# Kernel tuning notes

Hardware: AMD Instinct MI355X
Metric: run time of the kernel (lower is better)

## Reference

```python
import jax, jax.numpy as jnp
import numpy as np

SEQ_LEN = 256
E = 1024      # embedding_dim (= decoder LSTM hidden size)
H = 2048      # encoder hidden_dim
LAT = 512     # latent_space_dim
CLS = 512     # common_latent_space_dim
MIX = 384     # mixture_size
VJ = 64       # embedding_dim_VJ  (constraint: 2*VJ + LAT + MIX == E)
ALPH = 32; NVG = 64; NJG = 16
X_IDX = 0; B_IDX = 1  # indices of 'X' (start) and 'B' (stop) letters


def _lstm_final(xs, h0, c0, Wih, Whh, bih, bhh):
    """Run an LSTM over xs [T, B, in] and return the final hidden state [B, H]."""
    def step(carry, x):
        h, c = carry
        g = x @ Wih.T + bih + h @ Whh.T + bhh
        i, f, gg, o = jnp.split(g, 4, axis=-1)
        c = jax.nn.sigmoid(f) * c + jax.nn.sigmoid(i) * jnp.tanh(gg)
        h = jax.nn.sigmoid(o) * jnp.tanh(c)
        return (h, c), None
    (h, c), _ = jax.lax.scan(step, (h0, c0), xs)
    return h


def _decode(h0c, Wih, Whh, bih, bhh, start_vec, end_vec, n_steps):
    """Autoregressive LSTM decode: feed previous output back as next input.
    h0c [1,E] is used as both initial h and c (as in the source)."""
    def step(carry, _):
        h, c, prev = carry
        g = prev @ Wih.T + bih + h @ Whh.T + bhh
        i, f, gg, o = jnp.split(g, 4, axis=-1)
        c2 = jax.nn.sigmoid(f) * c + jax.nn.sigmoid(i) * jnp.tanh(gg)
        h2 = jax.nn.sigmoid(o) * jnp.tanh(c2)
        return (h2, c2, h2), h2
    _, ys = jax.lax.scan(step, (h0c, h0c, start_vec), None, length=n_steps)  # [T-2,1,E]
    seq = jnp.concatenate([start_vec[None], ys, end_vec[None]], axis=0)      # [T,1,E]
    return seq[::-1]  # source reverses the list before cat


def setup_inputs() -> dict:
    key = jax.random.key(0)
    ks = jax.random.split(key, 26)
    def g(k, shape):
        return jax.random.normal(k, shape, dtype=jnp.float32) * 0.05
    return {
        "x": jax.random.randint(ks[0], (SEQ_LEN,), 0, ALPH),
        "Vg": jax.random.randint(ks[1], (1,), 0, NVG),
        "Jg": jax.random.randint(ks[2], (1,), 0, NJG),
        "emb": g(ks[3], (ALPH, E)),
        "emb_Vg": g(ks[4], (NVG, VJ)),
        "emb_Jg": g(ks[5], (NJG, VJ)),
        "enc_Wih": g(ks[6], (4 * H, E)),
        "enc_Whh": g(ks[7], (4 * H, H)),
        "enc_bih": g(ks[8], (4 * H,)),
        "enc_bhh": g(ks[9], (4 * H,)),
        "cls_W": g(ks[10], (CLS, 2 * H)), "cls_b": g(ks[11], (CLS,)),
        "latf_W": g(ks[12], (LAT, H)), "latf_b": g(ks[13], (LAT,)),
        "latr_W": g(ks[14], (LAT, H)), "latr_b": g(ks[15], (LAT,)),
        "mix_W": g(ks[16], (MIX, CLS)), "mix_b": g(ks[17], (MIX,)),
        "recf_Wih": g(ks[18], (4 * E, E)), "recf_Whh": g(ks[19], (4 * E, E)),
        "recf_bih": g(ks[20], (4 * E,)), "recf_bhh": g(ks[21], (4 * E,)),
        "recr_Wih": g(ks[22], (4 * E, E)), "recr_Whh": g(ks[23], (4 * E, E)),
        "recr_bih": g(ks[24], (4 * E,)), "recr_bhh": g(ks[25], (4 * E,)),
    }


def reference(x, Vg, Jg, emb, emb_Vg, emb_Jg,
              enc_Wih, enc_Whh, enc_bih, enc_bhh,
              cls_W, cls_b, latf_W, latf_b, latr_W, latr_b,
              mix_W, mix_b,
              recf_Wih, recf_Whh, recf_bih, recf_bhh,
              recr_Wih, recr_Whh, recr_bih, recr_bhh):
    T = x.shape[0]
    emb_f = emb[x]          # [T, E]
    emb_r = emb_f[::-1]     # reversed sequence
    h0 = jnp.zeros((1, H), jnp.float32)
    # NB: the source (bug preserved) runs the reverse pass through lstm_in_f as well.
    hf = _lstm_final(emb_f[:, None, :], h0, h0, enc_Wih, enc_Whh, enc_bih, enc_bhh)  # [1,H]
    hr = _lstm_final(emb_r[:, None, :], h0, h0, enc_Wih, enc_Whh, enc_bih, enc_bhh)  # [1,H]
    # dropout treated in eval mode (identity) for a deterministic reference
    common = jnp.tanh(jnp.concatenate([hf, hr], axis=-1) @ cls_W.T + cls_b)  # [1,CLS]
    lat_f = hf @ latf_W.T + latf_b  # [1,LAT]
    lat_r = hr @ latr_W.T + latr_b
    vg = emb_Vg[Vg]  # [1,VJ]
    jg = emb_Jg[Jg]
    lat_f_full = jnp.concatenate([vg, lat_f, jg], axis=-1)  # [1, 2*VJ+LAT]
    lat_r_full = jnp.concatenate([vg, lat_r, jg], axis=-1)
    # source (bug preserved): mixture_to_f applied to both branches
    mix = common @ mix_W.T + mix_b                      # [1,MIX]
    h0f = jnp.concatenate([lat_f_full, mix], axis=-1)   # [1,E]
    h0r = jnp.concatenate([lat_r_full, mix], axis=-1)
    start = emb[X_IDX][None]  # 'X' embedding, [1,E]
    stop = emb[B_IDX][None]   # 'B' embedding
    rec_f = _decode(h0f, recf_Wih, recf_Whh, recf_bih, recf_bhh, start, stop, T - 2)
    rec_r = _decode(h0r, recr_Wih, recr_Whh, recr_bih, recr_bhh, stop, start, T - 2)
    return (lat_f_full[None], lat_r_full[None], rec_f, rec_r, emb_f, emb_r)
```

## Files before the change

### kernel.cpp

```cpp
#include <hip/hip_runtime.h>
#include <hip/hip_fp16.h>

#define NB 256
#define NT 512


struct KArgs {
  const int *x, *Vg, *Jg;
  const float *emb, *embVg, *embJg;
  const float *encWih, *encWhh, *encBih, *encBhh;
  const float *clsW, *clsB, *latfW, *latfB, *latrW, *latrB, *mixW, *mixB;
  const float *recWih[2], *recWhh[2], *recBih[2], *recBhh[2];
  float* out;
  unsigned* barFull;
  unsigned long long *eDat, *hTdec;
  float *common, *bsum, *d1, *embf, *P;
  unsigned short *Wcomb, *WhhE;
  int fast;
};

__device__ __forceinline__ unsigned packh2(float lo, float hi) {
  __half2 h = __floats2half2_rn(lo, hi);
  return *(unsigned*)&h;
}
__device__ __forceinline__ float2 h2f2(unsigned u) {
  __half2 h = *(__half2*)&u;
  return __half22float2(h);
}
__device__ __forceinline__ unsigned long long packtag(unsigned tag, float f) {
  return ((unsigned long long)tag << 32) | (unsigned long long)__float_as_uint(f);
}
__device__ __forceinline__ float sigm(float x) { return 1.f / (1.f + __expf(-x)); }
__device__ __forceinline__ float tanh_(float x) { return 2.f / (1.f + __expf(-2.f * x)) - 1.f; }
__device__ __forceinline__ float wred(float v) {
#pragma unroll
  for (int off = 32; off; off >>= 1) v += __shfl_xor(v, off, 64);
  return v;
}
__device__ __forceinline__ void cstoref(float* p, float v) {
  __hip_atomic_store(p, v, __ATOMIC_RELAXED, __HIP_MEMORY_SCOPE_AGENT);
}
__device__ __forceinline__ float cloadf(const float* p) {
  return __hip_atomic_load(p, __ATOMIC_RELAXED, __HIP_MEMORY_SCOPE_AGENT);
}
__device__ __forceinline__ void cstoreu(unsigned* p, unsigned v) {
  __hip_atomic_store(p, v, __ATOMIC_RELAXED, __HIP_MEMORY_SCOPE_AGENT);
}
__device__ __forceinline__ unsigned long long cload64(const unsigned long long* p) {
  return __hip_atomic_load(p, __ATOMIC_RELAXED, __HIP_MEMORY_SCOPE_AGENT);
}
__device__ __forceinline__ void cstore64(unsigned long long* p, unsigned long long v) {
  __hip_atomic_store(p, v, __ATOMIC_RELAXED, __HIP_MEMORY_SCOPE_AGENT);
}

__device__ __forceinline__ void gbar_tree(unsigned* tree, int idx, unsigned e) {
  const int ls = 8;
  __syncthreads();
  if (threadIdx.x == 0) {
    unsigned* leaf = tree + (idx >> 3) * ls;
    unsigned* root = tree + 32 * ls;
    unsigned* flag = root + ls;
    unsigned old = __hip_atomic_fetch_add(leaf, 1u, __ATOMIC_ACQ_REL, __HIP_MEMORY_SCOPE_AGENT);
    if (old == e * 8u - 1u) {
      unsigned ro = __hip_atomic_fetch_add(root, 1u, __ATOMIC_ACQ_REL, __HIP_MEMORY_SCOPE_AGENT);
      if (ro == e * 32u - 1u)
        __hip_atomic_store(flag, e, __ATOMIC_RELEASE, __HIP_MEMORY_SCOPE_AGENT);
    }
    while (__hip_atomic_load(flag, __ATOMIC_RELAXED, __HIP_MEMORY_SCOPE_AGENT) < e)
      __builtin_amdgcn_s_sleep(2);
    __builtin_amdgcn_fence(__ATOMIC_ACQUIRE, "agent");
  }
  __syncthreads();
}

__global__ __launch_bounds__(NT, 2) void rnn2_kernel(KArgs a) {
  __shared__ float smem[16384];
  const int tid = threadIdx.x;
  const int b = blockIdx.x;
  const int wq = __builtin_amdgcn_readfirstlane(tid >> 6);
  const int lane = tid & 63;

  float* out_recf = a.out + 1280;
  float* out_recr = a.out + 1280 + 262144;
  float* out_embf = a.out + 1280 + 2 * 262144;
  float* out_embr = a.out + 1280 + 3 * 262144;

  for (int i = tid; i < 2048; i += NT) smem[i] = a.emb[i];
  __syncthreads();
  {
    int wg = b * 8 + wq;
#pragma unroll 1
    for (int rr = 0; rr < 4; rr++) {
      int idx = wg + rr * 2048;
      int dir = idx >> 12;
      int row = idx & 4095;
      const float* Wih = a.recWih[dir];
      const float* sv = &smem[dir * 1024];
      float acc = 0.f;
#pragma unroll
      for (int kc = 0; kc < 4; kc++) {
        int k = kc * 256 + lane * 4;
        float4 wv = *(const float4*)&Wih[row * 1024 + k];
        float4 ev = *(const float4*)&sv[k];
        acc += wv.x * ev.x + wv.y * ev.y + wv.z * ev.z + wv.w * ev.w;
      }
      acc = wred(acc);
      if (lane == 0)
        cstoref(&a.d1[dir * 4096 + row], acc + a.recBih[dir][row] + a.recBhh[dir][row]);
    }
  }
  const int gtid = b * NT + tid;
  const int GSZ = NB * NT;
  for (int i = gtid; i < 256 * 1024; i += GSZ) {
    int t = i >> 10, e = i & 1023;
    float v = a.emb[a.x[t] * 1024 + e];
    cstoref(&a.embf[i], v);
    out_embf[i] = v;
    out_embr[(255 - t) * 1024 + e] = v;
  }
  if (gtid < 1024) {
    int e = gtid;
    out_recf[e] = a.emb[1024 + e];
    out_recf[255 * 1024 + e] = a.emb[e];
    out_recr[e] = a.emb[e];
    out_recr[255 * 1024 + e] = a.emb[1024 + e];
  }
  if (gtid < 2048) cstore64(&a.eDat[gtid], 0ULL);
  else if (gtid < 4096) cstore64(&a.eDat[gtid], 0x0000000100000001ULL);
  if (gtid < 4096) cstore64(&a.hTdec[gtid], packtag(0xFFFFFFFFu, 0.f));
  if (gtid < 8192) {
    int dir = gtid >> 12, r = gtid & 4095;
    cstoref(&a.bsum[gtid], a.recBih[dir][r] + a.recBhh[dir][r]);
  }
  if (a.fast) {
    unsigned* W32 = (unsigned*)a.WhhE;
    const int N4 = 8192 * 2048 / 4;
    for (int i = gtid; i < N4; i += GSZ) {
      float4 v = *(const float4*)&a.encWhh[(size_t)i * 4];
      cstoreu(&W32[i * 2], packh2(v.x, v.y));
      cstoreu(&W32[i * 2 + 1], packh2(v.z, v.w));
    }
    unsigned* C32 = (unsigned*)a.Wcomb;
    const int M4 = 4096 * 1024 / 4;
    for (int i = gtid; i < 2 * M4; i += GSZ) {
      int dir = (i >= M4) ? 1 : 0;
      int j = i - dir * M4;
      float4 va = *(const float4*)&a.recWih[dir][(size_t)j * 4];
      float4 vb = *(const float4*)&a.recWhh[dir][(size_t)j * 4];
      cstoreu(&C32[(size_t)dir * (M4 * 2) + j * 2], packh2(va.x + vb.x, va.y + vb.y));
      cstoreu(&C32[(size_t)dir * (M4 * 2) + j * 2 + 1], packh2(va.z + vb.z, va.w + vb.w));
    }
  }
  gbar_tree(a.barFull, b, 1u);

  {
    const int tdb = b & 7;
    const int rb = (b >> 3) * 256;
    const int td = tdb * 64 + lane;
    const int dirc = td >> 8;
    const int tcol = td & 255;
    float acc[2][16];
#pragma unroll
    for (int p = 0; p < 2; p++)
#pragma unroll
      for (int r = 0; r < 16; r++) acc[p][r] = 0.f;
    const int s_td = tid >> 3;
    const int s_j = tid & 7;
    int std_ = tdb * 64 + s_td;
    int st = std_ & 255;
    const float* s_esrc = &a.embf[((std_ >> 8) ? (255 - st) : st) * 1024];
#pragma unroll 1
    for (int kc = 0; kc < 4; kc++) {
      __syncthreads();
#pragma unroll
      for (int m = 0; m < 8; m++) {
        int kk = s_j * 32 + m * 4;
        float4 v = *(const float4*)&s_esrc[kc * 256 + kk];
        smem[(kk + 0) * 64 + s_td] = v.x;
        smem[(kk + 1) * 64 + s_td] = v.y;
        smem[(kk + 2) * 64 + s_td] = v.z;
        smem[(kk + 3) * 64 + s_td] = v.w;
      }
      __syncthreads();
#pragma unroll
      for (int p = 0; p < 2; p++) {
        int row0 = rb + wq * 32 + p * 16;
#pragma unroll 1
        for (int k4 = 0; k4 < 64; k4++) {
          float e0 = smem[(k4 * 4 + 0) * 64 + lane];
          float e1 = smem[(k4 * 4 + 1) * 64 + lane];
          float e2 = smem[(k4 * 4 + 2) * 64 + lane];
          float e3 = smem[(k4 * 4 + 3) * 64 + lane];
#pragma unroll
          for (int r = 0; r < 16; r++) {
            const float* wp = &a.encWih[(size_t)(row0 + r) * 1024 + kc * 256 + k4 * 4];
            float w0 = wp[0], w1 = wp[1], w2 = wp[2], w3 = wp[3];
            acc[p][r] = fmaf(e0, w0, fmaf(e1, w1, fmaf(e2, w2, fmaf(e3, w3, acc[p][r]))));
          }
        }
      }
    }
#pragma unroll
    for (int p = 0; p < 2; p++)
#pragma unroll
      for (int r = 0; r < 16; r++) {
        int row = rb + wq * 32 + p * 16 + r;
        float bias = a.encBih[row] + a.encBhh[row];
        cstoref(&a.P[(size_t)(dirc * 8192 + row) * 256 + tcol], acc[p][r] + bias);
      }
  }
  gbar_tree(a.barFull, b, 2u);

  {
    const int u = b * 8 + wq;
    float wreg[128];
    if (a.fast) {
      const unsigned long long* W64 = (const unsigned long long*)a.WhhE;
#pragma unroll
      for (int g = 0; g < 4; g++)
#pragma unroll
        for (int c = 0; c < 8; c++) {
          unsigned long long w = cload64(&W64[(size_t)(g * 2048 + u) * 512 + c * 64 + lane]);
          float2 f01 = h2f2((unsigned)w), f23 = h2f2((unsigned)(w >> 32));
          wreg[(g * 8 + c) * 4 + 0] = f01.x;
          wreg[(g * 8 + c) * 4 + 1] = f01.y;
          wreg[(g * 8 + c) * 4 + 2] = f23.x;
          wreg[(g * 8 + c) * 4 + 3] = f23.y;
        }
    }
    float cf = 0.f, cr = 0.f;
#pragma unroll 1
    for (int t = 0; t < 256; t++) {
      float pf[4], pr[4];
#pragma unroll
      for (int g = 0; g < 4; g++) {
        pf[g] = cloadf(&a.P[(size_t)(g * 2048 + u) * 256 + t]);
        pr[g] = cloadf(&a.P[(size_t)(8192 + g * 2048 + u) * 256 + t]);
      }
      {
        const unsigned long long* dp = a.eDat + (size_t)(t & 1) * 2048;
        const unsigned lo_e = (unsigned)t & 1u;
        const unsigned hi_e = ((unsigned)t >> 1) & 1u;
        unsigned long long v[4];
        for (;;) {
#pragma unroll
          for (int j = 0; j < 4; j++) v[j] = cload64(&dp[j * 512 + tid]);
          unsigned bad = 0;
#pragma unroll
          for (int j = 0; j < 4; j++)
            bad |= ((unsigned)v[j] ^ lo_e) | (((unsigned)(v[j] >> 32)) ^ hi_e);
          if (!(bad & 1u)) break;
          __builtin_amdgcn_s_sleep(1);
        }
#pragma unroll
        for (int j = 0; j < 4; j++) {
          smem[j * 512 + tid] = __uint_as_float((unsigned)v[j]);
          smem[2048 + j * 512 + tid] = __uint_as_float((unsigned)(v[j] >> 32));
        }
      }
      __syncthreads();
      float af[4] = {0, 0, 0, 0}, ar[4] = {0, 0, 0, 0};
      if (a.fast) {
#pragma unroll
        for (int c = 0; c < 8; c++) {
          float4 hf = *(const float4*)&smem[c * 256 + lane * 4];
          float4 hr = *(const float4*)&smem[2048 + c * 256 + lane * 4];
#pragma unroll
          for (int g = 0; g < 4; g++) {
            const int wb = (g * 8 + c) * 4;
            af[g] = fmaf(wreg[wb + 0], hf.x, fmaf(wreg[wb + 1], hf.y,
                    fmaf(wreg[wb + 2], hf.z, fmaf(wreg[wb + 3], hf.w, af[g]))));
            ar[g] = fmaf(wreg[wb + 0], hr.x, fmaf(wreg[wb + 1], hr.y,
                    fmaf(wreg[wb + 2], hr.z, fmaf(wreg[wb + 3], hr.w, ar[g]))));
          }
        }
      } else {
#pragma unroll 1
        for (int kc = 0; kc < 8; kc++) {
          int k = kc * 256 + lane * 4;
          float4 hf = *(const float4*)&smem[k];
          float4 hr = *(const float4*)&smem[2048 + k];
#pragma unroll
          for (int g = 0; g < 4; g++) {
            float4 wv = *(const float4*)&a.encWhh[(size_t)(g * 2048 + u) * 2048 + k];
            af[g] += wv.x * hf.x + wv.y * hf.y + wv.z * hf.z + wv.w * hf.w;
            ar[g] += wv.x * hr.x + wv.y * hr.y + wv.z * hr.z + wv.w * hr.w;
          }
        }
      }
#pragma unroll
      for (int g = 0; g < 4; g++) { af[g] = wred(af[g]); ar[g] = wred(ar[g]); }
      float gi = af[0] + pf[0], gf = af[1] + pf[1], gg = af[2] + pf[2], go = af[3] + pf[3];
      cf = sigm(gf) * cf + sigm(gi) * tanh_(gg);
      float hfv = sigm(go) * tanh_(cf);
      gi = ar[0] + pr[0]; gf = ar[1] + pr[1]; gg = ar[2] + pr[2]; go = ar[3] + pr[3];
      cr = sigm(gf) * cr + sigm(gi) * tanh_(gg);
      float hrv = sigm(go) * tanh_(cr);
      if (lane == 0) {
        unsigned tag = (unsigned)(t + 1);
        unsigned fa = (__float_as_uint(hfv) & ~1u) | (tag & 1u);
        unsigned fb = (__float_as_uint(hrv) & ~1u) | ((tag >> 1) & 1u);
        cstore64(&a.eDat[(size_t)((t + 1) & 1) * 2048 + u],
                 ((unsigned long long)fb << 32) | fa);
      }
      __syncthreads();
    }
  }

  if (b <= 192) {
    {
      const unsigned long long* dp = a.eDat;
      unsigned long long v[4];
      for (;;) {
#pragma unroll
        for (int j = 0; j < 4; j++) v[j] = cload64(&dp[j * 512 + tid]);
        unsigned bad = 0;
#pragma unroll
        for (int j = 0; j < 4; j++)
          bad |= (unsigned)v[j] | ((unsigned)(v[j] >> 32));
        if (!(bad & 1u)) break;
        __builtin_amdgcn_s_sleep(1);
      }
#pragma unroll
      for (int j = 0; j < 4; j++) {
        smem[j * 512 + tid] = __uint_as_float((unsigned)v[j]);
        smem[2048 + j * 512 + tid] = __uint_as_float((unsigned)(v[j] >> 32));
      }
    }
    __syncthreads();
    int wg = b * 8 + wq;
    if (wg < 512) {
      int r = wg;
      float acc = 0.f;
#pragma unroll 1
      for (int kc = 0; kc < 16; kc++) {
        int k = kc * 256 + lane * 4;
        float4 wv = *(const float4*)&a.clsW[(size_t)r * 4096 + k];
        float4 hv = *(const float4*)&smem[k];
        acc += wv.x * hv.x + wv.y * hv.y + wv.z * hv.z + wv.w * hv.w;
      }
      acc = wred(acc);
      if (lane == 0) cstoref(&a.common[r], tanh_(acc + a.clsB[r]));
    } else if (wg < 1024) {
      int r = wg - 512;
      float acc = 0.f;
#pragma unroll 1
      for (int kc = 0; kc < 8; kc++) {
        int k = kc * 256 + lane * 4;
        float4 wv = *(const float4*)&a.latfW[(size_t)r * 2048 + k];
        float4 hv = *(const float4*)&smem[k];
        acc += wv.x * hv.x + wv.y * hv.y + wv.z * hv.z + wv.w * hv.w;
      }
      acc = wred(acc);
      if (lane == 0) {
        float v = acc + a.latfB[r];
        cstore64(&a.hTdec[64 + r], packtag(0u, v));
        a.out[64 + r] = v;
      }
    } else if (wg < 1536) {
      int r = wg - 1024;
      float acc = 0.f;
#pragma unroll 1
      for (int kc = 0; kc < 8; kc++) {
        int k = kc * 256 + lane * 4;
        float4 wv = *(const float4*)&a.latrW[(size_t)r * 2048 + k];
        float4 hv = *(const float4*)&smem[2048 + k];
        acc += wv.x * hv.x + wv.y * hv.y + wv.z * hv.z + wv.w * hv.w;
      }
      acc = wred(acc);
      if (lane == 0) {
        float v = acc + a.latrB[r];
        cstore64(&a.hTdec[1024 + 64 + r], packtag(0u, v));
        a.out[640 + 64 + r] = v;
      }
    } else if (wg == 1536) {
      float v = a.embVg[a.Vg[0] * 64 + lane];
      cstore64(&a.hTdec[lane], packtag(0u, v));
      cstore64(&a.hTdec[1024 + lane], packtag(0u, v));
      a.out[lane] = v;
      a.out[640 + lane] = v;
    } else if (wg == 1537) {
      float v = a.embJg[a.Jg[0] * 64 + lane];
      cstore64(&a.hTdec[576 + lane], packtag(0u, v));
      cstore64(&a.hTdec[1024 + 576 + lane], packtag(0u, v));
      a.out[576 + lane] = v;
      a.out[640 + 576 + lane] = v;
    }
  }
  gbar_tree(a.barFull, b, 3u);
  if (b < 48) {
    int wg = b * 8 + wq;
    smem[tid] = cloadf(&a.common[tid]);
    __syncthreads();
    float acc = 0.f;
#pragma unroll
    for (int kc = 0; kc < 2; kc++) {
      int k = kc * 256 + lane * 4;
      float4 wv = *(const float4*)&a.mixW[(size_t)wg * 512 + k];
      float4 hv = *(const float4*)&smem[k];
      acc += wv.x * hv.x + wv.y * hv.y + wv.z * hv.z + wv.w * hv.w;
    }
    acc = wred(acc);
    if (lane == 0) {
      float v = acc + a.mixB[wg];
      cstore64(&a.hTdec[640 + wg], packtag(0u, v));
      cstore64(&a.hTdec[1024 + 640 + wg], packtag(0u, v));
    }
  }
  gbar_tree(a.barFull, b, 4u);

  {
    const int dir = b & 1;
    const int hidx = b >> 1;
    const int u = hidx * 8 + wq;
    float* outrec = dir ? out_recr : out_recf;
    float bs[4];
#pragma unroll
    for (int g = 0; g < 4; g++) bs[g] = cloadf(&a.bsum[dir * 4096 + g * 1024 + u]);
    float wd[64];
    if (a.fast) {
      const unsigned long long* C64 = (const unsigned long long*)a.Wcomb;
      const size_t dbase = (size_t)dir * (4096 * 1024 / 4);
#pragma unroll
      for (int g = 0; g < 4; g++)
#pragma unroll
        for (int c = 0; c < 4; c++) {
          unsigned long long w = cload64(&C64[dbase + (size_t)(g * 1024 + u) * 256 + c * 64 + lane]);
          float2 f01 = h2f2((unsigned)w), f23 = h2f2((unsigned)(w >> 32));
          wd[(g * 4 + c) * 4 + 0] = f01.x;
          wd[(g * 4 + c) * 4 + 1] = f01.y;
          wd[(g * 4 + c) * 4 + 2] = f23.x;
          wd[(g * 4 + c) * 4 + 3] = f23.y;
        }
    }
    float c = 0.f;
#pragma unroll 1
    for (int s = 1; s <= 254; s++) {
      {
        const unsigned long long* src = a.hTdec + ((s - 1) & 1) * 2048 + dir * 1024;
        const unsigned tg = (unsigned)(s - 1);
        unsigned long long v0, v1;
        for (;;) {
          v0 = cload64(&src[tid]);
          v1 = cload64(&src[512 + tid]);
          if ((((unsigned)(v0 >> 32)) ^ tg) == 0u && (((unsigned)(v1 >> 32)) ^ tg) == 0u) break;
          __builtin_amdgcn_s_sleep(1);
        }
        smem[tid] = __uint_as_float((unsigned)v0);
        smem[512 + tid] = __uint_as_float((unsigned)v1);
      }
      __syncthreads();
      float acc[4] = {0, 0, 0, 0};
      if (s == 1) {
        const float* Whh = a.recWhh[dir];
#pragma unroll 1
        for (int kc = 0; kc < 4; kc++) {
          int k = kc * 256 + lane * 4;
          float4 hv = *(const float4*)&smem[k];
#pragma unroll
          for (int g = 0; g < 4; g++) {
            float4 wv = *(const float4*)&Whh[(size_t)(g * 1024 + u) * 1024 + k];
            acc[g] += wv.x * hv.x + wv.y * hv.y + wv.z * hv.z + wv.w * hv.w;
          }
        }
      } else if (a.fast) {
#pragma unroll
        for (int cc = 0; cc < 4; cc++) {
          float4 hv = *(const float4*)&smem[cc * 256 + lane * 4];
#pragma unroll
          for (int g = 0; g < 4; g++) {
            const int wb = (g * 4 + cc) * 4;
            acc[g] = fmaf(wd[wb + 0], hv.x, fmaf(wd[wb + 1], hv.y,
                     fmaf(wd[wb + 2], hv.z, fmaf(wd[wb + 3], hv.w, acc[g]))));
          }
        }
      } else {
        const float* Wi = a.recWih[dir];
        const float* Wh = a.recWhh[dir];
#pragma unroll 1
        for (int kc = 0; kc < 4; kc++) {
          int k = kc * 256 + lane * 4;
          float4 hv = *(const float4*)&smem[k];
#pragma unroll
          for (int g = 0; g < 4; g++) {
            size_t ro = (size_t)(g * 1024 + u) * 1024 + k;
            float4 va = *(const float4*)&Wi[ro];
            float4 vb = *(const float4*)&Wh[ro];
            acc[g] += (va.x + vb.x) * hv.x + (va.y + vb.y) * hv.y +
                      (va.z + vb.z) * hv.z + (va.w + vb.w) * hv.w;
          }
        }
      }
#pragma unroll
      for (int g = 0; g < 4; g++) acc[g] = wred(acc[g]);
      float gi, gf, gg, go;
      if (s == 1) {
        gi = acc[0] + cloadf(&a.d1[dir * 4096 + u]);
        gf = acc[1] + cloadf(&a.d1[dir * 4096 + 1024 + u]);
        gg = acc[2] + cloadf(&a.d1[dir * 4096 + 2048 + u]);
        go = acc[3] + cloadf(&a.d1[dir * 4096 + 3072 + u]);
        c = smem[u];
      } else {
        gi = acc[0] + bs[0]; gf = acc[1] + bs[1]; gg = acc[2] + bs[2]; go = acc[3] + bs[3];
      }
      c = sigm(gf) * c + sigm(gi) * tanh_(gg);
      float h2 = sigm(go) * tanh_(c);
      if (lane == 0) {
        outrec[(size_t)(255 - s) * 1024 + u] = h2;
        if (s < 254)
          cstore64(&a.hTdec[(s & 1) * 2048 + dir * 1024 + u], packtag((unsigned)s, h2));
      }
      __syncthreads();
    }
  }
}

extern "C" void kernel_launch(void* const* d_in, const int* in_sizes, int n_in,
                              void* d_out, int out_size, void* d_ws, size_t ws_size,
                              hipStream_t stream) {
  (void)in_sizes; (void)n_in; (void)out_size;
  KArgs a;
  a.x = (const int*)d_in[0];
  a.Vg = (const int*)d_in[1];
  a.Jg = (const int*)d_in[2];
  a.emb = (const float*)d_in[3];
  a.embVg = (const float*)d_in[4];
  a.embJg = (const float*)d_in[5];
  a.encWih = (const float*)d_in[6];
  a.encWhh = (const float*)d_in[7];
  a.encBih = (const float*)d_in[8];
  a.encBhh = (const float*)d_in[9];
  a.clsW = (const float*)d_in[10];
  a.clsB = (const float*)d_in[11];
  a.latfW = (const float*)d_in[12];
  a.latfB = (const float*)d_in[13];
  a.latrW = (const float*)d_in[14];
  a.latrB = (const float*)d_in[15];
  a.mixW = (const float*)d_in[16];
  a.mixB = (const float*)d_in[17];
  a.recWih[0] = (const float*)d_in[18];
  a.recWhh[0] = (const float*)d_in[19];
  a.recBih[0] = (const float*)d_in[20];
  a.recBhh[0] = (const float*)d_in[21];
  a.recWih[1] = (const float*)d_in[22];
  a.recWhh[1] = (const float*)d_in[23];
  a.recBih[1] = (const float*)d_in[24];
  a.recBhh[1] = (const float*)d_in[25];
  a.out = (float*)d_out;
  char* ws = (char*)d_ws;
  a.barFull = (unsigned*)ws;
  a.eDat = (unsigned long long*)(ws + 4096);
  a.hTdec = (unsigned long long*)(ws + 36864);
  a.common = (float*)(ws + 69632);
  a.bsum = (float*)(ws + 71680);
  a.d1 = (float*)(ws + 104448);
  a.embf = (float*)(ws + 137216);
  a.P = (float*)(ws + 1204224);
  a.Wcomb = (unsigned short*)(ws + 17981440);
  a.WhhE = (unsigned short*)(ws + 34758656);
  a.fast = (ws_size >= 68313088ULL) ? 1 : 0;
  hipMemsetAsync(ws, 0, 4096, stream);
  hipLaunchKernelGGL(rnn2_kernel, dim3(NB), dim3(NT), 0, stream, a);
}
```

Baseline: 2.511 ms.

## Embed 2-bit step tags in float mantissas and vectorize spin-wait polling

Replaces the separate 32-bit tag words in the decoder exchange buffer with a 2-bit step tag stored in the low mantissa bits of each hidden value. This halves the polled data and lets each thread read contiguous chunks. Encoder polling now uses two 16-byte loads per thread with an inline-asm sc1 path, and skips polling at t=0. Decoder output stores are deferred by one step so they stay off the critical path between publish and wait. The cost is a small precision loss in the hidden values exchanged between blocks (the low 2 mantissa bits are overwritten).

After: 2.700 ms. 7.5% more time.

```diff
diff --git a/kernel.cpp b/kernel.cpp
--- a/kernel.cpp
+++ b/kernel.cpp
@@ -4,6 +4,8 @@
 #define NB 256
 #define NT 512
 
+
+typedef unsigned u32x4 __attribute__((ext_vector_type(4)));
 
 struct KArgs {
   const int *x, *Vg, *Jg;
@@ -13,8 +15,8 @@
   const float *recWih[2], *recWhh[2], *recBih[2], *recBhh[2];
   float* out;
   unsigned* barFull;
-  unsigned long long *eDat, *hTdec;
-  float *common, *bsum, *d1, *embf, *P;
+  unsigned long long* eDat;
+  float *hDec, *common, *bsum, *d1, *embf, *P;
   unsigned short *Wcomb, *WhhE;
   int fast;
 };
@@ -27,9 +29,6 @@
   __half2 h = *(__half2*)&u;
   return __half22float2(h);
 }
-__device__ __forceinline__ unsigned long long packtag(unsigned tag, float f) {
-  return ((unsigned long long)tag << 32) | (unsigned long long)__float_as_uint(f);
-}
 __device__ __forceinline__ float sigm(float x) { return 1.f / (1.f + __expf(-x)); }
 __device__ __forceinline__ float tanh_(float x) { return 2.f / (1.f + __expf(-2.f * x)) - 1.f; }
 __device__ __forceinline__ float wred(float v) {
@@ -51,6 +50,15 @@
 }
 __device__ __forceinline__ void cstore64(unsigned long long* p, unsigned long long v) {
   __hip_atomic_store(p, v, __ATOMIC_RELAXED, __HIP_MEMORY_SCOPE_AGENT);
+}
+__device__ __forceinline__ void cload32B(const void* p, u32x4& A, u32x4& B) {
+  asm volatile(
+      "global_load_dwordx4 %0, %2, off sc1\n\t"
+      "global_load_dwordx4 %1, %2, off offset:16 sc1\n\t"
+      "s_waitcnt vmcnt(0)"
+      : "=&v"(A), "=&v"(B)
+      : "v"(p)
+      : "memory");
 }
 
 __device__ __forceinline__ void gbar_tree(unsigned* tree, int idx, unsigned e) {
@@ -125,9 +133,8 @@
     out_recr[e] = a.emb[e];
     out_recr[255 * 1024 + e] = a.emb[1024 + e];
   }
-  if (gtid < 2048) cstore64(&a.eDat[gtid], 0ULL);
-  else if (gtid < 4096) cstore64(&a.eDat[gtid], 0x0000000100000001ULL);
-  if (gtid < 4096) cstore64(&a.hTdec[gtid], packtag(0xFFFFFFFFu, 0.f));
+  if (gtid < 4096) cstore64(&a.eDat[gtid], 0x0000000300000003ULL);
+  if (gtid < 4096) cstoreu((unsigned*)a.hDec + gtid, 3u);
   if (gtid < 8192) {
     int dir = gtid >> 12, r = gtid & 4095;
     cstoref(&a.bsum[gtid], a.recBih[dir][r] + a.recBhh[dir][r]);
@@ -237,26 +244,27 @@
         pf[g] = cloadf(&a.P[(size_t)(g * 2048 + u) * 256 + t]);
         pr[g] = cloadf(&a.P[(size_t)(8192 + g * 2048 + u) * 256 + t]);
       }
-      {
-        const unsigned long long* dp = a.eDat + (size_t)(t & 1) * 2048;
-        const unsigned lo_e = (unsigned)t & 1u;
-        const unsigned hi_e = ((unsigned)t >> 1) & 1u;
-        unsigned long long v[4];
+      if (t == 0) {
+#pragma unroll
+        for (int j = 0; j < 8; j++) smem[j * 512 + tid] = 0.f;
+      } else {
+        const char* dp = (const char*)(a.eDat + (size_t)(t & 1) * 2048) + 32 * tid;
+        const unsigned tg2 = (unsigned)t & 3u;
+        u32x4 A, B;
         for (;;) {
-#pragma unroll
-          for (int j = 0; j < 4; j++) v[j] = cload64(&dp[j * 512 + tid]);
-          unsigned bad = 0;
-#pragma unroll
-          for (int j = 0; j < 4; j++)
-            bad |= ((unsigned)v[j] ^ lo_e) | (((unsigned)(v[j] >> 32)) ^ hi_e);
-          if (!(bad & 1u)) break;
+          cload32B(dp, A, B);
+          unsigned bad = (A.x ^ tg2) | (A.y ^ tg2) | (A.z ^ tg2) | (A.w ^ tg2) |
+                         (B.x ^ tg2) | (B.y ^ tg2) | (B.z ^ tg2) | (B.w ^ tg2);
+          if (!(bad & 3u)) break;
           __builtin_amdgcn_s_sleep(1);
         }
-#pragma unroll
-        for (int j = 0; j < 4; j++) {
-          smem[j * 512 + tid] = __uint_as_float((unsigned)v[j]);
-          smem[2048 + j * 512 + tid] = __uint_as_float((unsigned)(v[j] >> 32));
-        }
+        float4 sf, sr;
+        sf.x = __uint_as_float(A.x); sr.x = __uint_as_float(A.y);
+        sf.y = __uint_as_float(A.z); sr.y = __uint_as_float(A.w);
+        sf.z = __uint_as_float(B.x); sr.z = __uint_as_float(B.y);
+        sf.w = __uint_as_float(B.z); sr.w = __uint_as_float(B.w);
+        *(float4*)&smem[4 * tid] = sf;
+        *(float4*)&smem[2048 + 4 * tid] = sr;
       }
       __syncthreads();
       float af[4] = {0, 0, 0, 0}, ar[4] = {0, 0, 0, 0};
@@ -297,9 +305,9 @@
       cr = sigm(gf) * cr + sigm(gi) * tanh_(gg);
       float hrv = sigm(go) * tanh_(cr);
       if (lane == 0) {
-        unsigned tag = (unsigned)(t + 1);
-        unsigned fa = (__float_as_uint(hfv) & ~1u) | (tag & 1u);
-        unsigned fb = (__float_as_uint(hrv) & ~1u) | ((tag >> 1) & 1u);
+        unsigned tag = (unsigned)(t + 1) & 3u;
+        unsigned fa = (__float_as_uint(hfv) & ~3u) | tag;
+        unsigned fb = (__float_as_uint(hrv) & ~3u) | tag;
         cstore64(&a.eDat[(size_t)((t + 1) & 1) * 2048 + u],
                  ((unsigned long long)fb << 32) | fa);
       }
@@ -309,23 +317,21 @@
 
   if (b <= 192) {
     {
-      const unsigned long long* dp = a.eDat;
-      unsigned long long v[4];
+      const char* dp = (const char*)a.eDat + 32 * tid;
+      u32x4 A, B;
       for (;;) {
-#pragma unroll
-        for (int j = 0; j < 4; j++) v[j] = cload64(&dp[j * 512 + tid]);
-        unsigned bad = 0;
-#pragma unroll
-        for (int j = 0; j < 4; j++)
-          bad |= (unsigned)v[j] | ((unsigned)(v[j] >> 32));
-        if (!(bad & 1u)) break;
+        cload32B(dp, A, B);
+        unsigned bad = A.x | A.y | A.z | A.w | B.x | B.y | B.z | B.w;
+        if (!(bad & 3u)) break;
         __builtin_amdgcn_s_sleep(1);
       }
-#pragma unroll
-      for (int j = 0; j < 4; j++) {
-        smem[j * 512 + tid] = __uint_as_float((unsigned)v[j]);
-        smem[2048 + j * 512 + tid] = __uint_as_float((unsigned)(v[j] >> 32));
-      }
+      float4 sf, sr;
+      sf.x = __uint_as_float(A.x); sr.x = __uint_as_float(A.y);
+      sf.y = __uint_as_float(A.z); sr.y = __uint_as_float(A.w);
+      sf.z = __uint_as_float(B.x); sr.z = __uint_as_float(B.y);
+      sf.w = __uint_as_float(B.z); sr.w = __uint_as_float(B.w);
+      *(float4*)&smem[4 * tid] = sf;
+      *(float4*)&smem[2048 + 4 * tid] = sr;
     }
     __syncthreads();
     int wg = b * 8 + wq;
@@ -354,7 +360,7 @@
       acc = wred(acc);
       if (lane == 0) {
         float v = acc + a.latfB[r];
-        cstore64(&a.hTdec[64 + r], packtag(0u, v));
+        cstoref(&a.hDec[64 + r], __uint_as_float(__float_as_uint(v) & ~3u));
         a.out[64 + r] = v;
       }
     } else if (wg < 1536) {
@@ -370,19 +376,21 @@
       acc = wred(acc);
       if (lane == 0) {
         float v = acc + a.latrB[r];
-        cstore64(&a.hTdec[1024 + 64 + r], packtag(0u, v));
+        cstoref(&a.hDec[1024 + 64 + r], __uint_as_float(__float_as_uint(v) & ~3u));
         a.out[640 + 64 + r] = v;
       }
     } else if (wg == 1536) {
       float v = a.embVg[a.Vg[0] * 64 + lane];
-      cstore64(&a.hTdec[lane], packtag(0u, v));
-      cstore64(&a.hTdec[1024 + lane], packtag(0u, v));
+      float tv = __uint_as_float(__float_as_uint(v) & ~3u);
+      cstoref(&a.hDec[lane], tv);
+      cstoref(&a.hDec[1024 + lane], tv);
       a.out[lane] = v;
       a.out[640 + lane] = v;
     } else if (wg == 1537) {
       float v = a.embJg[a.Jg[0] * 64 + lane];
-      cstore64(&a.hTdec[576 + lane], packtag(0u, v));
-      cstore64(&a.hTdec[1024 + 576 + lane], packtag(0u, v));
+      float tv = __uint_as_float(__float_as_uint(v) & ~3u);
+      cstoref(&a.hDec[576 + lane], tv);
+      cstoref(&a.hDec[1024 + 576 + lane], tv);
       a.out[576 + lane] = v;
       a.out[640 + 576 + lane] = v;
     }
@@ -403,8 +411,9 @@
     acc = wred(acc);
     if (lane == 0) {
       float v = acc + a.mixB[wg];
-      cstore64(&a.hTdec[640 + wg], packtag(0u, v));
-      cstore64(&a.hTdec[1024 + 640 + wg], packtag(0u, v));
+      float tv = __uint_as_float(__float_as_uint(v) & ~3u);
+      cstoref(&a.hDec[640 + wg], tv);
+      cstoref(&a.hDec[1024 + 640 + wg], tv);
     }
   }
   gbar_tree(a.barFull, b, 4u);
@@ -433,22 +442,26 @@
           wd[(g * 4 + c) * 4 + 3] = f23.y;
         }
     }
-    float c = 0.f;
+    float c = 0.f, h2p = 0.f;
 #pragma unroll 1
     for (int s = 1; s <= 254; s++) {
       {
-        const unsigned long long* src = a.hTdec + ((s - 1) & 1) * 2048 + dir * 1024;
-        const unsigned tg = (unsigned)(s - 1);
-        unsigned long long v0, v1;
+        const unsigned long long* src =
+            (const unsigned long long*)(a.hDec + ((s - 1) & 1) * 2048 + dir * 1024);
+        const unsigned tg2 = (unsigned)(s - 1) & 3u;
+        unsigned long long v;
         for (;;) {
-          v0 = cload64(&src[tid]);
-          v1 = cload64(&src[512 + tid]);
-          if ((((unsigned)(v0 >> 32)) ^ tg) == 0u && (((unsigned)(v1 >> 32)) ^ tg) == 0u) break;
+          v = cload64(&src[tid]);
+          unsigned bad = ((unsigned)v ^ tg2) | (((unsigned)(v >> 32)) ^ tg2);
+          if (!(bad & 3u)) break;
           __builtin_amdgcn_s_sleep(1);
         }
-        smem[tid] = __uint_as_float((unsigned)v0);
-        smem[512 + tid] = __uint_as_float((unsigned)v1);
-      }
+        float2 sv;
+        sv.x = __uint_as_float((unsigned)v);
+        sv.y = __uint_as_float((unsigned)(v >> 32));
+        *(float2*)&smem[2 * tid] = sv;
+      }
+      if (lane == 0 && s > 1) outrec[(size_t)(255 - (s - 1)) * 1024 + u] = h2p;
       __syncthreads();
       float acc[4] = {0, 0, 0, 0};
       if (s == 1) {
@@ -505,13 +518,14 @@
       }
       c = sigm(gf) * c + sigm(gi) * tanh_(gg);
       float h2 = sigm(go) * tanh_(c);
-      if (lane == 0) {
-        outrec[(size_t)(255 - s) * 1024 + u] = h2;
-        if (s < 254)
-          cstore64(&a.hTdec[(s & 1) * 2048 + dir * 1024 + u], packtag((unsigned)s, h2));
-      }
+      if (lane == 0 && s < 254) {
+        cstoref(&a.hDec[(s & 1) * 2048 + dir * 1024 + u],
+                __uint_as_float((__float_as_uint(h2) & ~3u) | ((unsigned)s & 3u)));
+      }
+      h2p = h2;
       __syncthreads();
     }
+    if (lane == 0) outrec[(size_t)(255 - 254) * 1024 + u] = h2p;
   }
 }
 
@@ -550,7 +564,7 @@
   char* ws = (char*)d_ws;
   a.barFull = (unsigned*)ws;
   a.eDat = (unsigned long long*)(ws + 4096);
-  a.hTdec = (unsigned long long*)(ws + 36864);
+  a.hDec = (float*)(ws + 36864);
   a.common = (float*)(ws + 69632);
   a.bsum = (float*)(ws + 71680);
   a.d1 = (float*)(ws + 104448);
```

## Compute encoder input projections per block locally and share forward/reverse results

Applied to the files above, without the earlier changes.

The input-projection pre-pass now has each block compute only the gate rows it later consumes in the recurrent loop (its 8 units times 4 gates) for all 256 timesteps, writing into a block-private slice of P. The reverse direction reuses the forward projection by indexing 255-t, since the reverse sequence is the forward one reversed, which halves the projection work. Recurrent-loop reads of P become normal loads of block-local, likely cache-resident data instead of coherent loads from a global layout. The trade-off is less register blocking in the GEMM (4 accumulators instead of 32), so weight reuse per shared-memory tile drops.

New measurement: 2.146 ms. -14.6%, faster.

```diff
diff --git a/kernel.cpp b/kernel.cpp
--- a/kernel.cpp
+++ b/kernel.cpp
@@ -154,37 +154,26 @@
   gbar_tree(a.barFull, b, 1u);
 
   {
-    const int tdb = b & 7;
-    const int rb = (b >> 3) * 256;
-    const int td = tdb * 64 + lane;
-    const int dirc = td >> 8;
-    const int tcol = td & 255;
-    float acc[2][16];
-#pragma unroll
-    for (int p = 0; p < 2; p++)
-#pragma unroll
-      for (int r = 0; r < 16; r++) acc[p][r] = 0.f;
+    float* Pp = a.P + (size_t)b * 8192;
     const int s_td = tid >> 3;
     const int s_j = tid & 7;
-    int std_ = tdb * 64 + s_td;
-    int st = std_ & 255;
-    const float* s_esrc = &a.embf[((std_ >> 8) ? (255 - st) : st) * 1024];
-#pragma unroll 1
-    for (int kc = 0; kc < 4; kc++) {
-      __syncthreads();
-#pragma unroll
-      for (int m = 0; m < 8; m++) {
-        int kk = s_j * 32 + m * 4;
-        float4 v = *(const float4*)&s_esrc[kc * 256 + kk];
-        smem[(kk + 0) * 64 + s_td] = v.x;
-        smem[(kk + 1) * 64 + s_td] = v.y;
-        smem[(kk + 2) * 64 + s_td] = v.z;
-        smem[(kk + 3) * 64 + s_td] = v.w;
-      }
-      __syncthreads();
-#pragma unroll
-      for (int p = 0; p < 2; p++) {
-        int row0 = rb + wq * 32 + p * 16;
+#pragma unroll 1
+    for (int tc = 0; tc < 4; tc++) {
+      float acc[4] = {0.f, 0.f, 0.f, 0.f};
+      const float* esrc = &a.embf[(size_t)(tc * 64 + s_td) * 1024];
+#pragma unroll 1
+      for (int kc = 0; kc < 4; kc++) {
+        __syncthreads();
+#pragma unroll
+        for (int m = 0; m < 8; m++) {
+          int kk = s_j * 32 + m * 4;
+          float4 v = *(const float4*)&esrc[kc * 256 + kk];
+          smem[(kk + 0) * 64 + s_td] = v.x;
+          smem[(kk + 1) * 64 + s_td] = v.y;
+          smem[(kk + 2) * 64 + s_td] = v.z;
+          smem[(kk + 3) * 64 + s_td] = v.w;
+        }
+        __syncthreads();
 #pragma unroll 1
         for (int k4 = 0; k4 < 64; k4++) {
           float e0 = smem[(k4 * 4 + 0) * 64 + lane];
@@ -192,27 +181,24 @@
           float e2 = smem[(k4 * 4 + 2) * 64 + lane];
           float e3 = smem[(k4 * 4 + 3) * 64 + lane];
 #pragma unroll
-          for (int r = 0; r < 16; r++) {
-            const float* wp = &a.encWih[(size_t)(row0 + r) * 1024 + kc * 256 + k4 * 4];
-            float w0 = wp[0], w1 = wp[1], w2 = wp[2], w3 = wp[3];
-            acc[p][r] = fmaf(e0, w0, fmaf(e1, w1, fmaf(e2, w2, fmaf(e3, w3, acc[p][r]))));
+          for (int g = 0; g < 4; g++) {
+            const float* wp = &a.encWih[(size_t)(g * 2048 + b * 8 + wq) * 1024 + kc * 256 + k4 * 4];
+            acc[g] = fmaf(e0, wp[0], fmaf(e1, wp[1], fmaf(e2, wp[2], fmaf(e3, wp[3], acc[g]))));
           }
         }
       }
-    }
-#pragma unroll
-    for (int p = 0; p < 2; p++)
-#pragma unroll
-      for (int r = 0; r < 16; r++) {
-        int row = rb + wq * 32 + p * 16 + r;
-        float bias = a.encBih[row] + a.encBhh[row];
-        cstoref(&a.P[(size_t)(dirc * 8192 + row) * 256 + tcol], acc[p][r] + bias);
-      }
+#pragma unroll
+      for (int g = 0; g < 4; g++) {
+        int row = g * 2048 + b * 8 + wq;
+        Pp[(g * 8 + wq) * 256 + tc * 64 + lane] = acc[g] + a.encBih[row] + a.encBhh[row];
+      }
+    }
   }
   gbar_tree(a.barFull, b, 2u);
 
   {
     const int u = b * 8 + wq;
+    const float* Pp = a.P + (size_t)b * 8192;
     float wreg[128];
     if (a.fast) {
       const unsigned long long* W64 = (const unsigned long long*)a.WhhE;
@@ -234,8 +220,8 @@
       float pf[4], pr[4];
 #pragma unroll
       for (int g = 0; g < 4; g++) {
-        pf[g] = cloadf(&a.P[(size_t)(g * 2048 + u) * 256 + t]);
-        pr[g] = cloadf(&a.P[(size_t)(8192 + g * 2048 + u) * 256 + t]);
+        pf[g] = Pp[(g * 8 + wq) * 256 + t];
+        pr[g] = Pp[(g * 8 + wq) * 256 + 255 - t];
       }
       {
         const unsigned long long* dp = a.eDat + (size_t)(t & 1) * 2048;
```
